# Optimization experiments

Hardware: AMD Instinct MI355X
Metric: run time of the kernel (lower is better)

The kernel has to match this reference:

```python
import jax, jax.numpy as jnp
import numpy as np

B, C, H, W = 32, 192, 32, 32
CH, STRIDE = 8, 2
FEAT = CH * (H // STRIDE) * (W // STRIDE)  # 8*16*16 = 2048


def setup_inputs() -> dict:
    key = jax.random.key(0)
    ks = jax.random.split(key, 7)
    inp = jax.random.normal(ks[0], (B, C, H, W), jnp.float32)
    w_left_out = jax.random.normal(ks[1], (B, C, H, W), jnp.float32)
    conv_w = jax.random.normal(ks[2], (CH, C, 3, 3), jnp.float32) * 0.05
    conv_b = jnp.zeros((CH,), jnp.float32)
    # small scale keeps diag(U) moderate so exp(s) stays finite
    lin_w = jax.random.normal(ks[3], (C * C, FEAT), jnp.float32) * 0.01
    lin_b = jax.random.normal(ks[4], (C * C,), jnp.float32) * 0.1
    s_sign = jnp.sign(jax.random.normal(ks[5], (C,), jnp.float32))
    return dict(inp=inp, w_left_out=w_left_out, conv_w=conv_w, conv_b=conv_b,
                lin_w=lin_w, lin_b=lin_b, s_sign=s_sign)


def _cond_net(x, conv_w, conv_b, lin_w, lin_b):
    # Conv2d(C->CH, k=3, stride=2, pad=1) + ReLU + Flatten + Linear(FEAT -> C*C)
    h = jax.lax.conv_general_dilated(
        x, conv_w, window_strides=(STRIDE, STRIDE), padding=((1, 1), (1, 1)),
        dimension_numbers=('NCHW', 'OIHW', 'NCHW'))
    h = jax.nn.relu(h + conv_b[None, :, None, None])
    return h.reshape(x.shape[0], -1) @ lin_w.T + lin_b  # [B, C*C]


def reference(inp, w_left_out, conv_w, conv_b, lin_w, lin_b, s_sign):
    b, c, height, width = inp.shape
    cond = _cond_net(w_left_out, conv_w, conv_b, lin_w, lin_b)
    mats = cond.reshape(b, c, c)
    # batched LU: a = p @ l @ u (scipy convention, unit-diag l)
    p, l, u = jax.vmap(jax.scipy.linalg.lu)(mats)
    s = jnp.diagonal(u, axis1=1, axis2=2)          # [B, C] raw diag(U)
    eye = jnp.eye(c, dtype=inp.dtype)
    l_full = jnp.tril(l, -1) + eye                  # l * l_mask + I
    u_full = jnp.triu(u, 1) + (s_sign[None, :] * jnp.exp(s))[..., None] * eye
    weight = p @ l_full @ u_full                    # [B, C, C]
    # batched 1x1 conv == per-sample GEMM over spatial positions
    out = jnp.einsum('bij,bjhw->bihw', weight, inp)
    log_w = jnp.mean(jnp.sum(s, axis=1))            # sum(w_s) averaged over batch
    log_det = (height * width) * log_w
    return out, log_det
```

## Files before the change

kernel.cpp:

```cpp
#include <hip/hip_runtime.h>
#include <math.h>


#define NFEAT 2048
#define NN    36864

__global__ __launch_bounds__(256) void conv_kernel(const float* __restrict__ w,
                                                   const float* __restrict__ cw,
                                                   float* __restrict__ hpart) {
  int blk = blockIdx.x;
  int b = blk >> 2, cs = blk & 3;
  int tid = threadIdx.x;
  int oy = tid >> 4, ox = tid & 15;
  __shared__ float wlds[8 * 48 * 9];
  for (int idx = tid; idx < 8 * 48 * 9; idx += 256) {
    int ch = idx / 432, rem = idx - ch * 432;
    int c = rem / 9, kk = rem - c * 9;
    wlds[idx] = cw[ch * 1728 + (cs * 48 + c) * 9 + kk];
  }
  __syncthreads();
  float acc[8];
#pragma unroll
  for (int ch = 0; ch < 8; ++ch) acc[ch] = 0.f;
  const float* img0 = w + (((size_t)b * 192 + cs * 48) << 10);
  for (int c = 0; c < 48; ++c) {
    const float* img = img0 + ((size_t)c << 10);
    float iv[9];
#pragma unroll
    for (int ky = 0; ky < 3; ++ky)
#pragma unroll
      for (int kx = 0; kx < 3; ++kx) {
        int iy = 2 * oy - 1 + ky, ix = 2 * ox - 1 + kx;
        bool ok = (iy >= 0) & (iy < 32) & (ix >= 0) & (ix < 32);
        iv[ky * 3 + kx] = ok ? img[iy * 32 + ix] : 0.f;
      }
#pragma unroll
    for (int ch = 0; ch < 8; ++ch) {
      const float* wp = &wlds[(ch * 48 + c) * 9];
      float s = acc[ch];
#pragma unroll
      for (int t = 0; t < 9; ++t) s = fmaf(iv[t], wp[t], s);
      acc[ch] = s;
    }
  }
  size_t base = ((size_t)(cs * 32 + b) << 11) + tid;
#pragma unroll
  for (int ch = 0; ch < 8; ++ch) hpart[base + (ch << 8)] = acc[ch];
}

__global__ __launch_bounds__(256) void hreduce_kernel(const float* __restrict__ hpart,
                                                      const float* __restrict__ cb,
                                                      float* __restrict__ h_bt) {
  int g = blockIdx.x * 256 + threadIdx.x;
  int k = g & 2047, b = g >> 11;
  float s = 0.f;
#pragma unroll
  for (int cs = 0; cs < 4; ++cs) s += hpart[(((size_t)(cs * 32 + b)) << 11) + k];
  s += cb[k >> 8];
  s = fmaxf(s, 0.f);
  h_bt[g] = s;
}

#define WROW(r) ((r) * 68 + (((r) >> 3) << 2))
__global__ __launch_bounds__(128) void linear_kernel(const float* __restrict__ h_bt,
                                                     const float* __restrict__ lw,
                                                     float* __restrict__ qpart) {
  __shared__ float Wbuf[8768];
  __shared__ float Hbuf[2192];
  int tid = threadIdx.x;
  int blk = blockIdx.x;
  int q = blk & 3;
  int tile = blk >> 2;
  int n0 = tile << 7;
  int kqb = q << 9;
  int bp = tid & 7;
  int ng = tid >> 3;
  int nb = ng << 3;
  int bb0 = bp << 2;
  float acc[32];
#pragma unroll
  for (int i = 0; i < 32; ++i) acc[i] = 0.f;

  for (int kc = 0; kc < 8; ++kc) {
    int koff = kqb + (kc << 6);
#pragma unroll
    for (int j = 0; j < 16; ++j) {
      int f = tid + (j << 7);
      int row = f >> 4, c4 = (f & 15) << 2;
      *(float4*)(Wbuf + WROW(row) + c4) =
          *(const float4*)(lw + (size_t)(n0 + row) * 2048 + koff + c4);
    }
#pragma unroll
    for (int j = 0; j < 4; ++j) {
      int f = tid + (j << 7);
      int bi = f >> 4, c4 = (f & 15) << 2;
      *(float4*)(Hbuf + WROW(bi) + c4) =
          *(const float4*)(h_bt + (size_t)bi * 2048 + koff + c4);
    }
    __syncthreads();
#pragma unroll 2
    for (int k4 = 0; k4 < 16; ++k4) {
      int kk = k4 << 2;
      float4 h0 = *(const float4*)(Hbuf + WROW(bb0 + 0) + kk);
      float4 h1 = *(const float4*)(Hbuf + WROW(bb0 + 1) + kk);
      float4 h2 = *(const float4*)(Hbuf + WROW(bb0 + 2) + kk);
      float4 h3 = *(const float4*)(Hbuf + WROW(bb0 + 3) + kk);
#pragma unroll
      for (int j = 0; j < 8; ++j) {
        float4 w4 = *(const float4*)(Wbuf + WROW(nb + j) + kk);
        float s0 = acc[j * 4 + 0], s1 = acc[j * 4 + 1];
        float s2 = acc[j * 4 + 2], s3 = acc[j * 4 + 3];
        s0 = fmaf(w4.x, h0.x, s0); s0 = fmaf(w4.y, h0.y, s0);
        s0 = fmaf(w4.z, h0.z, s0); s0 = fmaf(w4.w, h0.w, s0);
        s1 = fmaf(w4.x, h1.x, s1); s1 = fmaf(w4.y, h1.y, s1);
        s1 = fmaf(w4.z, h1.z, s1); s1 = fmaf(w4.w, h1.w, s1);
        s2 = fmaf(w4.x, h2.x, s2); s2 = fmaf(w4.y, h2.y, s2);
        s2 = fmaf(w4.z, h2.z, s2); s2 = fmaf(w4.w, h2.w, s2);
        s3 = fmaf(w4.x, h3.x, s3); s3 = fmaf(w4.y, h3.y, s3);
        s3 = fmaf(w4.z, h3.z, s3); s3 = fmaf(w4.w, h3.w, s3);
        acc[j * 4 + 0] = s0; acc[j * 4 + 1] = s1;
        acc[j * 4 + 2] = s2; acc[j * 4 + 3] = s3;
      }
    }
    __syncthreads();
  }
#pragma unroll
  for (int i = 0; i < 4; ++i) {
    float* p = qpart + (size_t)q * 1179648 + (size_t)(bb0 + i) * NN + n0 + nb;
    *(float4*)(p + 0) = make_float4(acc[0 * 4 + i], acc[1 * 4 + i], acc[2 * 4 + i], acc[3 * 4 + i]);
    *(float4*)(p + 4) = make_float4(acc[4 * 4 + i], acc[5 * 4 + i], acc[6 * 4 + i], acc[7 * 4 + i]);
  }
}

__global__ __launch_bounds__(256) void combine_kernel(const float* __restrict__ qpart,
                                                      const float* __restrict__ lb,
                                                      float* __restrict__ mats) {
  int blk = blockIdx.x;
  int b = blk / 18, nt = blk - b * 18;
  int n = (nt << 11) + (threadIdx.x << 3);
  size_t base = (size_t)b * NN + n;
#pragma unroll
  for (int h = 0; h < 2; ++h) {
    float4 q0 = *(const float4*)(qpart + 0 * 1179648 + base + 4 * h);
    float4 q1 = *(const float4*)(qpart + 1 * 1179648 + base + 4 * h);
    float4 q2 = *(const float4*)(qpart + 2 * 1179648 + base + 4 * h);
    float4 q3 = *(const float4*)(qpart + 3 * 1179648 + base + 4 * h);
    float4 bb = *(const float4*)(lb + n + 4 * h);
    float4 o;
    o.x = ((q0.x + q1.x) + q2.x) + q3.x + bb.x;
    o.y = ((q0.y + q1.y) + q2.y) + q3.y + bb.y;
    o.z = ((q0.z + q1.z) + q2.z) + q3.z + bb.z;
    o.w = ((q0.w + q1.w) + q2.w) + q3.w + bb.w;
    *(float4*)(mats + base + 4 * h) = o;
  }
}

#define CAT_(A, B) A##B
#define CAT(A, B) CAT_(A, B)
#define PR_0(R) CAT(pA, R).x
#define PR_1(R) CAT(pA, R).y
#define PR_2(R) CAT(pA, R).z
#define PR_3(R) CAT(pA, R).w
#define PR_4(R) CAT(pB, R).x
#define PR_5(R) CAT(pB, R).y
#define PR_6(R) CAT(pB, R).z
#define PR_7(R) CAT(pB, R).w
#define PR(R, K) CAT(PR_, K)(R)
#define UU_0 uA.x
#define UU_1 uA.y
#define UU_2 uA.z
#define UU_3 uA.w
#define UU_4 uB.x
#define UU_5 uB.y
#define UU_6 uB.z
#define UU_7 uB.w
#define UU(K) CAT(UU_, K)
#define UPDJ(R, J) PR(R, J) = fmaf(-m, UU(J), PR(R, J));
#define TAIL_0(R) UPDJ(R,1) UPDJ(R,2) UPDJ(R,3) UPDJ(R,4) UPDJ(R,5) UPDJ(R,6) UPDJ(R,7)
#define TAIL_1(R) UPDJ(R,2) UPDJ(R,3) UPDJ(R,4) UPDJ(R,5) UPDJ(R,6) UPDJ(R,7)
#define TAIL_2(R) UPDJ(R,3) UPDJ(R,4) UPDJ(R,5) UPDJ(R,6) UPDJ(R,7)
#define TAIL_3(R) UPDJ(R,4) UPDJ(R,5) UPDJ(R,6) UPDJ(R,7)
#define TAIL_4(R) UPDJ(R,5) UPDJ(R,6) UPDJ(R,7)
#define TAIL_5(R) UPDJ(R,6) UPDJ(R,7)
#define TAIL_6(R) UPDJ(R,7)
#define TAIL_7(R)
#define UPDROW(R, KK, kg)                                                      \
  if (CAT(lg, R) > (kg)) {                                                     \
    float m = PR(R, KK) * recip;                                               \
    PR(R, KK) = m;                                                             \
    CAT(TAIL_, KK)(R)                                                          \
  }
#define PSTEP(KK) {                                                            \
  const int kg = kpP + KK;                                                     \
  float bv = -1.f; int br = 0x7fffffff;                                        \
  { float v = fabsf(PR(0,KK)); if (lg0 >= kg && (v > bv || (v == bv && lg0 < br))) { bv = v; br = lg0; } } \
  { float v = fabsf(PR(1,KK)); if (lg1 >= kg && (v > bv || (v == bv && lg1 < br))) { bv = v; br = lg1; } } \
  { float v = fabsf(PR(2,KK)); if (lg2 >= kg && (v > bv || (v == bv && lg2 < br))) { bv = v; br = lg2; } } \
  for (int msk = 1; msk <= 32; msk <<= 1) {                                    \
    float ov = __shfl_xor(bv, msk, 64);                                        \
    int obr = __shfl_xor(br, msk, 64);                                         \
    if (ov > bv || (ov == bv && obr < br)) { bv = ov; br = obr; }              \
  }                                                                            \
  bool own0 = (lg0 == br), own1 = (lg1 == br), own2 = (lg2 == br);             \
  float4 sA = own1 ? pA1 : (own2 ? pA2 : pA0);                                 \
  float4 sB = own1 ? pB1 : (own2 ? pB2 : pB0);                                 \
  int owner = (int)__ffsll(__ballot(own0 | own1 | own2)) - 1;                  \
  float4 uA, uB;                                                               \
  uA.x = __shfl(sA.x, owner); uA.y = __shfl(sA.y, owner);                      \
  uA.z = __shfl(sA.z, owner); uA.w = __shfl(sA.w, owner);                      \
  uB.x = __shfl(sB.x, owner); uB.y = __shfl(sB.y, owner);                      \
  uB.z = __shfl(sB.z, owner); uB.w = __shfl(sB.w, owner);                      \
  float piv = UU(KK);                                                          \
  float recip = 1.0f / piv;                                                    \
  if (tid == 0) {                                                              \
    diagU[kg] = piv;                                                           \
    int t0 = rowmap[kg], t1 = rowmap[br];                                      \
    rowmap[kg] = t1; rowmap[br] = t0;                                          \
  }                                                                            \
  lg0 = (lg0 == kg) ? br : ((lg0 == br) ? kg : lg0);                           \
  lg1 = (lg1 == kg) ? br : ((lg1 == br) ? kg : lg1);                           \
  lg2 = (lg2 == kg) ? br : ((lg2 == br) ? kg : lg2);                           \
  UPDROW(0, KK, kg)                                                            \
  UPDROW(1, KK, kg)                                                            \
  UPDROW(2, KK, kg)                                                            \
}
#define FMA4(D, M, S) {                                                        \
  float mm = (M);                                                              \
  D.x = fmaf(-mm, S.x, D.x); D.y = fmaf(-mm, S.y, D.y);                        \
  D.z = fmaf(-mm, S.z, D.z); D.w = fmaf(-mm, S.w, D.w);                        \
}
#define PANEL(KPV) {                                                           \
  const int kpP = (KPV);                                                       \
  const int pcP = kpP >> 2;                                                    \
  float4 pA0 = As4[tid * 49 + pcP],         pB0 = As4[tid * 49 + pcP + 1];     \
  float4 pA1 = As4[(tid + 64) * 49 + pcP],  pB1 = As4[(tid + 64) * 49 + pcP + 1]; \
  float4 pA2 = As4[(tid + 128) * 49 + pcP], pB2 = As4[(tid + 128) * 49 + pcP + 1]; \
  PSTEP(0) PSTEP(1) PSTEP(2) PSTEP(3) PSTEP(4) PSTEP(5) PSTEP(6) PSTEP(7)     \
  As4[tid * 49 + pcP] = pA0;         As4[tid * 49 + pcP + 1] = pB0;            \
  As4[(tid + 64) * 49 + pcP] = pA1;  As4[(tid + 64) * 49 + pcP + 1] = pB1;     \
  As4[(tid + 128) * 49 + pcP] = pA2; As4[(tid + 128) * 49 + pcP + 1] = pB2;    \
}

__global__ __launch_bounds__(768, 1) void lu_kernel(float* __restrict__ A0,
                                                    const float* __restrict__ ssign,
                                                    float* __restrict__ ssum) {
  __shared__ float4 As4[192 * 49];
  __shared__ int rowmap[192];
  __shared__ float diagU[192];
  __shared__ float4 dval4[48];
  float* dvalf = (float*)dval4;
  int b = blockIdx.x;
  int tid = threadIdx.x;
  float* __restrict__ A = A0 + (size_t)b * NN;

#pragma unroll
  for (int j = 0; j < 12; ++j) {
    int chunk = tid + 768 * j;
    int row = chunk / 48, q = chunk - row * 48;
    As4[row * 49 + q] = *(const float4*)(A + row * 192 + 4 * q);
  }
  for (int i = tid; i < 192; i += 768) rowmap[i] = i;
  __syncthreads();

  int lg0 = tid, lg1 = tid + 64, lg2 = tid + 128;

  if (tid < 64) { PANEL(0) }
  __syncthreads();

  const int qg = tid >> 4;
  const int slot = tid & 15;

  for (int p = 0; p < 23; ++p) {
    const int kp = p << 3;
    const int pc = kp >> 2;
    const int qp1 = pc + 2;

    if (tid >= qp1 && tid < 48) {
      const int q = tid;
      const int ur0 = rowmap[kp + 0], ur1 = rowmap[kp + 1];
      const int ur2 = rowmap[kp + 2], ur3 = rowmap[kp + 3];
      const int ur4 = rowmap[kp + 4], ur5 = rowmap[kp + 5];
      const int ur6 = rowmap[kp + 6], ur7 = rowmap[kp + 7];
      float4 u40 = As4[ur0 * 49 + q], u41 = As4[ur1 * 49 + q];
      float4 u42 = As4[ur2 * 49 + q], u43 = As4[ur3 * 49 + q];
      float4 u44 = As4[ur4 * 49 + q], u45 = As4[ur5 * 49 + q];
      float4 u46 = As4[ur6 * 49 + q], u47 = As4[ur7 * 49 + q];
      { float4 la = As4[ur1 * 49 + pc];
        FMA4(u41, la.x, u40) }
      { float4 la = As4[ur2 * 49 + pc];
        FMA4(u42, la.x, u40) FMA4(u42, la.y, u41) }
      { float4 la = As4[ur3 * 49 + pc];
        FMA4(u43, la.x, u40) FMA4(u43, la.y, u41) FMA4(u43, la.z, u42) }
      { float4 la = As4[ur4 * 49 + pc];
        FMA4(u44, la.x, u40) FMA4(u44, la.y, u41) FMA4(u44, la.z, u42) FMA4(u44, la.w, u43) }
      { float4 la = As4[ur5 * 49 + pc]; float4 lb2 = As4[ur5 * 49 + pc + 1];
        FMA4(u45, la.x, u40) FMA4(u45, la.y, u41) FMA4(u45, la.z, u42) FMA4(u45, la.w, u43)
        FMA4(u45, lb2.x, u44) }
      { float4 la = As4[ur6 * 49 + pc]; float4 lb2 = As4[ur6 * 49 + pc + 1];
        FMA4(u46, la.x, u40) FMA4(u46, la.y, u41) FMA4(u46, la.z, u42) FMA4(u46, la.w, u43)
        FMA4(u46, lb2.x, u44) FMA4(u46, lb2.y, u45) }
      { float4 la = As4[ur7 * 49 + pc]; float4 lb2 = As4[ur7 * 49 + pc + 1];
        FMA4(u47, la.x, u40) FMA4(u47, la.y, u41) FMA4(u47, la.z, u42) FMA4(u47, la.w, u43)
        FMA4(u47, lb2.x, u44) FMA4(u47, lb2.y, u45) FMA4(u47, lb2.z, u46) }
      As4[ur0 * 49 + q] = u40; As4[ur1 * 49 + q] = u41;
      As4[ur2 * 49 + q] = u42; As4[ur3 * 49 + q] = u43;
      As4[ur4 * 49 + q] = u44; As4[ur5 * 49 + q] = u45;
      As4[ur6 * 49 + q] = u46; As4[ur7 * 49 + q] = u47;
    }
    __syncthreads();

    {
      const int col = qp1 + (tid >= 384 ? 1 : 0);
      const int rsl = tid - (tid >= 384 ? 384 : 0);
      const int s = kp + 8 + rsl;
      if (s < 192) {
        const int ua0 = rowmap[kp + 0], ua1 = rowmap[kp + 1];
        const int ua2 = rowmap[kp + 2], ua3 = rowmap[kp + 3];
        const int ua4 = rowmap[kp + 4], ua5 = rowmap[kp + 5];
        const int ua6 = rowmap[kp + 6], ua7 = rowmap[kp + 7];
        float4 u40 = As4[ua0 * 49 + col], u41 = As4[ua1 * 49 + col];
        float4 u42 = As4[ua2 * 49 + col], u43 = As4[ua3 * 49 + col];
        float4 u44 = As4[ua4 * 49 + col], u45 = As4[ua5 * 49 + col];
        float4 u46 = As4[ua6 * 49 + col], u47 = As4[ua7 * 49 + col];
        int phys = rowmap[s];
        float4 la = As4[phys * 49 + pc];
        float4 lb2 = As4[phys * 49 + pc + 1];
        float4 c = As4[phys * 49 + col];
        FMA4(c, la.x, u40) FMA4(c, la.y, u41) FMA4(c, la.z, u42) FMA4(c, la.w, u43)
        FMA4(c, lb2.x, u44) FMA4(c, lb2.y, u45) FMA4(c, lb2.z, u46) FMA4(c, lb2.w, u47)
        As4[phys * 49 + col] = c;
      }
    }
    int php0, php1, php2, php3, php4, php5, php6, php7, php8, php9, php10, php11;
#define SNAP(I) CAT(php, I) = rowmap[slot + (I << 4)];
    SNAP(0) SNAP(1) SNAP(2) SNAP(3) SNAP(4) SNAP(5) SNAP(6)
    SNAP(7) SNAP(8) SNAP(9) SNAP(10) SNAP(11)
#undef SNAP
    __syncthreads();

    if (tid < 64) {
      PANEL(kp + 8)
    } else if (qg >= qp1 + 2) {
      const int q = qg;
      const int ub0 = rowmap[kp + 0], ub1 = rowmap[kp + 1];
      const int ub2 = rowmap[kp + 2], ub3 = rowmap[kp + 3];
      const int ub4 = rowmap[kp + 4], ub5 = rowmap[kp + 5];
      const int ub6 = rowmap[kp + 6], ub7 = rowmap[kp + 7];
      float4 u40 = As4[ub0 * 49 + q], u41 = As4[ub1 * 49 + q];
      float4 u42 = As4[ub2 * 49 + q], u43 = As4[ub3 * 49 + q];
      float4 u44 = As4[ub4 * 49 + q], u45 = As4[ub5 * 49 + q];
      float4 u46 = As4[ub6 * 49 + q], u47 = As4[ub7 * 49 + q];
#define GEMMROW(I) {                                                           \
      int s = slot + (I << 4);                                                 \
      if (s >= kp + 8) {                                                       \
        int phys = CAT(php, I);                                                \
        float4 la = As4[phys * 49 + pc];                                       \
        float4 lb2 = As4[phys * 49 + pc + 1];                                  \
        float4 c = As4[phys * 49 + q];                                         \
        FMA4(c, la.x, u40) FMA4(c, la.y, u41) FMA4(c, la.z, u42) FMA4(c, la.w, u43) \
        FMA4(c, lb2.x, u44) FMA4(c, lb2.y, u45) FMA4(c, lb2.z, u46) FMA4(c, lb2.w, u47) \
        As4[phys * 49 + q] = c;                                                \
      }                                                                        \
    }
      GEMMROW(0) GEMMROW(1) GEMMROW(2) GEMMROW(3) GEMMROW(4) GEMMROW(5)
      GEMMROW(6) GEMMROW(7) GEMMROW(8) GEMMROW(9) GEMMROW(10) GEMMROW(11)
#undef GEMMROW
    }
    __syncthreads();
  }

  if (tid == 0) {
    float s = 0.f;
    for (int i = 0; i < 192; ++i) s += diagU[i];
    ssum[b] = s;
  }
  if (tid < 192) dvalf[tid] = ssign[tid] * expf(diagU[tid]) - diagU[tid];
  __syncthreads();
  {
    const int r = tid >> 2;
    const int tq = tid & 3;
    int i = r;
    int phys = rowmap[r];
    float di = dvalf[i];
    float* __restrict__ G = A + (size_t)phys * 192;
    int qi = i >> 2;
    for (int j = 0; j < 12; ++j) {
      int q = tq + 4 * j;
      if (q > qi) continue;
      float4 g4 = *(float4*)(G + 4 * q);
      float4 a4 = As4[phys * 49 + q];
      float4 d4 = dval4[q];
      if (q == qi) {
        int c0 = 4 * q;
        g4.x = (c0 + 0 < i) ? g4.x + a4.x * d4.x : ((c0 + 0 == i) ? g4.x + di : g4.x);
        g4.y = (c0 + 1 < i) ? g4.y + a4.y * d4.y : ((c0 + 1 == i) ? g4.y + di : g4.y);
        g4.z = (c0 + 2 < i) ? g4.z + a4.z * d4.z : ((c0 + 2 == i) ? g4.z + di : g4.z);
        g4.w = (c0 + 3 < i) ? g4.w + a4.w * d4.w : ((c0 + 3 == i) ? g4.w + di : g4.w);
      } else {
        g4.x += a4.x * d4.x;
        g4.y += a4.y * d4.y;
        g4.z += a4.z * d4.z;
        g4.w += a4.w * d4.w;
      }
      *(float4*)(G + 4 * q) = g4;
    }
  }
}

__global__ __launch_bounds__(256) void out_kernel(const float* __restrict__ wt,
                                                  const float* __restrict__ inp,
                                                  const float* __restrict__ ssum,
                                                  float* __restrict__ out) {
  int blk = blockIdx.x;
  int b = blk / 24, rem = blk % 24;
  int it = rem >> 3, jt = rem & 7;
  int i0 = it << 6, hw0 = jt << 7;
  int tid = threadIdx.x;
  int tx = tid & 31, ty = tid >> 5;
  __shared__ float wlds[64 * 36];
  __shared__ float xlds[32 * 128];
  const float* wb = wt + (size_t)b * NN;
  const float* xb = inp + (((size_t)b * 192) << 10);
  float acc[8][4];
#pragma unroll
  for (int r = 0; r < 8; ++r)
#pragma unroll
    for (int c = 0; c < 4; ++c) acc[r][c] = 0.f;
  for (int kc = 0; kc < 6; ++kc) {
    __syncthreads();
#pragma unroll
    for (int j = 0; j < 2; ++j) {
      int f4 = tid + (j << 8);
      int row = f4 >> 3, c4 = (f4 & 7) << 2;
      float4 v = *(const float4*)(wb + (size_t)(i0 + row) * 192 + (kc << 5) + c4);
      *(float4*)(wlds + row * 36 + c4) = v;
    }
#pragma unroll
    for (int j = 0; j < 4; ++j) {
      int f4 = tid + (j << 8);
      int row = f4 >> 5, c4 = (f4 & 31) << 2;
      float4 v = *(const float4*)(xb + (((size_t)(kc << 5) + row) << 10) + hw0 + c4);
      *(float4*)(xlds + (row << 7) + c4) = v;
    }
    __syncthreads();
#pragma unroll 4
    for (int k = 0; k < 32; ++k) {
      float4 xv = *(const float4*)(xlds + (k << 7) + (tx << 2));
      float wr[8];
#pragma unroll
      for (int r = 0; r < 8; ++r) wr[r] = wlds[(ty * 8 + r) * 36 + k];
#pragma unroll
      for (int r = 0; r < 8; ++r) {
        acc[r][0] = fmaf(wr[r], xv.x, acc[r][0]);
        acc[r][1] = fmaf(wr[r], xv.y, acc[r][1]);
        acc[r][2] = fmaf(wr[r], xv.z, acc[r][2]);
        acc[r][3] = fmaf(wr[r], xv.w, acc[r][3]);
      }
    }
  }
  float* ob = out + (((size_t)b * 192 + i0 + ty * 8) << 10) + hw0 + (tx << 2);
#pragma unroll
  for (int r = 0; r < 8; ++r) {
    float4 v = make_float4(acc[r][0], acc[r][1], acc[r][2], acc[r][3]);
    *(float4*)(ob + ((size_t)r << 10)) = v;
  }
  if (blk == 0 && tid == 0) {
    float s = 0.f;
    for (int i = 0; i < 32; ++i) s += ssum[i];
    out[6291456] = 32.f * s;
  }
}

extern "C" void kernel_launch(void* const* d_in, const int* in_sizes, int n_in,
                              void* d_out, int out_size, void* d_ws, size_t ws_size,
                              hipStream_t stream) {
  const float* inp = (const float*)d_in[0];
  const float* wlo = (const float*)d_in[1];
  const float* cw  = (const float*)d_in[2];
  const float* cb  = (const float*)d_in[3];
  const float* lw  = (const float*)d_in[4];
  const float* lb  = (const float*)d_in[5];
  const float* ss  = (const float*)d_in[6];
  float* out = (float*)d_out;
  float* ws = (float*)d_ws;
  float* hpart = ws;
  float* h_bt  = ws + 262144;
  float* mats  = ws + 327680;
  float* ssum  = ws + 1507328;
  float* qpart = out;
  hipLaunchKernelGGL(conv_kernel,    dim3(128),  dim3(256), 0, stream, wlo, cw, hpart);
  hipLaunchKernelGGL(hreduce_kernel, dim3(256),  dim3(256), 0, stream, hpart, cb, h_bt);
  hipLaunchKernelGGL(linear_kernel,  dim3(1152), dim3(128), 0, stream, h_bt, lw, qpart);
  hipLaunchKernelGGL(combine_kernel, dim3(576),  dim3(256), 0, stream, qpart, lb, mats);
  hipLaunchKernelGGL(lu_kernel,      dim3(32),   dim3(768), 0, stream, mats, ss, ssum);
  hipLaunchKernelGGL(out_kernel,     dim3(768),  dim3(256), 0, stream, mats, inp, ssum, out);
}
```

Measured before the change: 424.4 us.

## Widen blocked LU panel from 8 to 16 columns

```diff
diff --git a/kernel.cpp b/kernel.cpp
--- a/kernel.cpp
+++ b/kernel.cpp
@@ -157,45 +157,69 @@
 
 #define CAT_(A, B) A##B
 #define CAT(A, B) CAT_(A, B)
-#define PR_0(R) CAT(pA, R).x
-#define PR_1(R) CAT(pA, R).y
-#define PR_2(R) CAT(pA, R).z
-#define PR_3(R) CAT(pA, R).w
-#define PR_4(R) CAT(pB, R).x
-#define PR_5(R) CAT(pB, R).y
-#define PR_6(R) CAT(pB, R).z
-#define PR_7(R) CAT(pB, R).w
-#define PR(R, K) CAT(PR_, K)(R)
-#define UU_0 uA.x
-#define UU_1 uA.y
-#define UU_2 uA.z
-#define UU_3 uA.w
-#define UU_4 uB.x
-#define UU_5 uB.y
-#define UU_6 uB.z
-#define UU_7 uB.w
-#define UU(K) CAT(UU_, K)
-#define UPDJ(R, J) PR(R, J) = fmaf(-m, UU(J), PR(R, J));
-#define TAIL_0(R) UPDJ(R,1) UPDJ(R,2) UPDJ(R,3) UPDJ(R,4) UPDJ(R,5) UPDJ(R,6) UPDJ(R,7)
-#define TAIL_1(R) UPDJ(R,2) UPDJ(R,3) UPDJ(R,4) UPDJ(R,5) UPDJ(R,6) UPDJ(R,7)
-#define TAIL_2(R) UPDJ(R,3) UPDJ(R,4) UPDJ(R,5) UPDJ(R,6) UPDJ(R,7)
-#define TAIL_3(R) UPDJ(R,4) UPDJ(R,5) UPDJ(R,6) UPDJ(R,7)
-#define TAIL_4(R) UPDJ(R,5) UPDJ(R,6) UPDJ(R,7)
-#define TAIL_5(R) UPDJ(R,6) UPDJ(R,7)
-#define TAIL_6(R) UPDJ(R,7)
-#define TAIL_7(R)
-#define UPDROW(R, KK, kg)                                                      \
+#define PR16_0(R)  CAT(pA, R).x
+#define PR16_1(R)  CAT(pA, R).y
+#define PR16_2(R)  CAT(pA, R).z
+#define PR16_3(R)  CAT(pA, R).w
+#define PR16_4(R)  CAT(pB, R).x
+#define PR16_5(R)  CAT(pB, R).y
+#define PR16_6(R)  CAT(pB, R).z
+#define PR16_7(R)  CAT(pB, R).w
+#define PR16_8(R)  CAT(pC, R).x
+#define PR16_9(R)  CAT(pC, R).y
+#define PR16_10(R) CAT(pC, R).z
+#define PR16_11(R) CAT(pC, R).w
+#define PR16_12(R) CAT(pD, R).x
+#define PR16_13(R) CAT(pD, R).y
+#define PR16_14(R) CAT(pD, R).z
+#define PR16_15(R) CAT(pD, R).w
+#define PR16(R, K) CAT(PR16_, K)(R)
+#define UU16_0  uA.x
+#define UU16_1  uA.y
+#define UU16_2  uA.z
+#define UU16_3  uA.w
+#define UU16_4  uB.x
+#define UU16_5  uB.y
+#define UU16_6  uB.z
+#define UU16_7  uB.w
+#define UU16_8  uC.x
+#define UU16_9  uC.y
+#define UU16_10 uC.z
+#define UU16_11 uC.w
+#define UU16_12 uD.x
+#define UU16_13 uD.y
+#define UU16_14 uD.z
+#define UU16_15 uD.w
+#define UU16(K) CAT(UU16_, K)
+#define UPDJ16(R, J) PR16(R, J) = fmaf(-m, UU16(J), PR16(R, J));
+#define T16_0(R)  UPDJ16(R,1) UPDJ16(R,2) UPDJ16(R,3) UPDJ16(R,4) UPDJ16(R,5) UPDJ16(R,6) UPDJ16(R,7) UPDJ16(R,8) UPDJ16(R,9) UPDJ16(R,10) UPDJ16(R,11) UPDJ16(R,12) UPDJ16(R,13) UPDJ16(R,14) UPDJ16(R,15)
+#define T16_1(R)  UPDJ16(R,2) UPDJ16(R,3) UPDJ16(R,4) UPDJ16(R,5) UPDJ16(R,6) UPDJ16(R,7) UPDJ16(R,8) UPDJ16(R,9) UPDJ16(R,10) UPDJ16(R,11) UPDJ16(R,12) UPDJ16(R,13) UPDJ16(R,14) UPDJ16(R,15)
+#define T16_2(R)  UPDJ16(R,3) UPDJ16(R,4) UPDJ16(R,5) UPDJ16(R,6) UPDJ16(R,7) UPDJ16(R,8) UPDJ16(R,9) UPDJ16(R,10) UPDJ16(R,11) UPDJ16(R,12) UPDJ16(R,13) UPDJ16(R,14) UPDJ16(R,15)
+#define T16_3(R)  UPDJ16(R,4) UPDJ16(R,5) UPDJ16(R,6) UPDJ16(R,7) UPDJ16(R,8) UPDJ16(R,9) UPDJ16(R,10) UPDJ16(R,11) UPDJ16(R,12) UPDJ16(R,13) UPDJ16(R,14) UPDJ16(R,15)
+#define T16_4(R)  UPDJ16(R,5) UPDJ16(R,6) UPDJ16(R,7) UPDJ16(R,8) UPDJ16(R,9) UPDJ16(R,10) UPDJ16(R,11) UPDJ16(R,12) UPDJ16(R,13) UPDJ16(R,14) UPDJ16(R,15)
+#define T16_5(R)  UPDJ16(R,6) UPDJ16(R,7) UPDJ16(R,8) UPDJ16(R,9) UPDJ16(R,10) UPDJ16(R,11) UPDJ16(R,12) UPDJ16(R,13) UPDJ16(R,14) UPDJ16(R,15)
+#define T16_6(R)  UPDJ16(R,7) UPDJ16(R,8) UPDJ16(R,9) UPDJ16(R,10) UPDJ16(R,11) UPDJ16(R,12) UPDJ16(R,13) UPDJ16(R,14) UPDJ16(R,15)
+#define T16_7(R)  UPDJ16(R,8) UPDJ16(R,9) UPDJ16(R,10) UPDJ16(R,11) UPDJ16(R,12) UPDJ16(R,13) UPDJ16(R,14) UPDJ16(R,15)
+#define T16_8(R)  UPDJ16(R,9) UPDJ16(R,10) UPDJ16(R,11) UPDJ16(R,12) UPDJ16(R,13) UPDJ16(R,14) UPDJ16(R,15)
+#define T16_9(R)  UPDJ16(R,10) UPDJ16(R,11) UPDJ16(R,12) UPDJ16(R,13) UPDJ16(R,14) UPDJ16(R,15)
+#define T16_10(R) UPDJ16(R,11) UPDJ16(R,12) UPDJ16(R,13) UPDJ16(R,14) UPDJ16(R,15)
+#define T16_11(R) UPDJ16(R,12) UPDJ16(R,13) UPDJ16(R,14) UPDJ16(R,15)
+#define T16_12(R) UPDJ16(R,13) UPDJ16(R,14) UPDJ16(R,15)
+#define T16_13(R) UPDJ16(R,14) UPDJ16(R,15)
+#define T16_14(R) UPDJ16(R,15)
+#define T16_15(R)
+#define UPDROW16(R, KK, kg)                                                    \
   if (CAT(lg, R) > (kg)) {                                                     \
-    float m = PR(R, KK) * recip;                                               \
-    PR(R, KK) = m;                                                             \
-    CAT(TAIL_, KK)(R)                                                          \
-  }
-#define PSTEP(KK) {                                                            \
+    float m = PR16(R, KK) * recip;                                             \
+    PR16(R, KK) = m;                                                           \
+    CAT(T16_, KK)(R)                                                           \
+  }
+#define PSTEP16(KK) {                                                          \
   const int kg = kpP + KK;                                                     \
   float bv = -1.f; int br = 0x7fffffff;                                        \
-  { float v = fabsf(PR(0,KK)); if (lg0 >= kg && (v > bv || (v == bv && lg0 < br))) { bv = v; br = lg0; } } \
-  { float v = fabsf(PR(1,KK)); if (lg1 >= kg && (v > bv || (v == bv && lg1 < br))) { bv = v; br = lg1; } } \
-  { float v = fabsf(PR(2,KK)); if (lg2 >= kg && (v > bv || (v == bv && lg2 < br))) { bv = v; br = lg2; } } \
+  { float v = fabsf(PR16(0,KK)); if (lg0 >= kg && (v > bv || (v == bv && lg0 < br))) { bv = v; br = lg0; } } \
+  { float v = fabsf(PR16(1,KK)); if (lg1 >= kg && (v > bv || (v == bv && lg1 < br))) { bv = v; br = lg1; } } \
+  { float v = fabsf(PR16(2,KK)); if (lg2 >= kg && (v > bv || (v == bv && lg2 < br))) { bv = v; br = lg2; } } \
   for (int msk = 1; msk <= 32; msk <<= 1) {                                    \
     float ov = __shfl_xor(bv, msk, 64);                                        \
     int obr = __shfl_xor(br, msk, 64);                                         \
@@ -204,13 +228,19 @@
   bool own0 = (lg0 == br), own1 = (lg1 == br), own2 = (lg2 == br);             \
   float4 sA = own1 ? pA1 : (own2 ? pA2 : pA0);                                 \
   float4 sB = own1 ? pB1 : (own2 ? pB2 : pB0);                                 \
+  float4 sC = own1 ? pC1 : (own2 ? pC2 : pC0);                                 \
+  float4 sD = own1 ? pD1 : (own2 ? pD2 : pD0);                                 \
   int owner = (int)__ffsll(__ballot(own0 | own1 | own2)) - 1;                  \
-  float4 uA, uB;                                                               \
+  float4 uA, uB, uC, uD;                                                       \
   uA.x = __shfl(sA.x, owner); uA.y = __shfl(sA.y, owner);                      \
   uA.z = __shfl(sA.z, owner); uA.w = __shfl(sA.w, owner);                      \
   uB.x = __shfl(sB.x, owner); uB.y = __shfl(sB.y, owner);                      \
   uB.z = __shfl(sB.z, owner); uB.w = __shfl(sB.w, owner);                      \
-  float piv = UU(KK);                                                          \
+  uC.x = __shfl(sC.x, owner); uC.y = __shfl(sC.y, owner);                      \
+  uC.z = __shfl(sC.z, owner); uC.w = __shfl(sC.w, owner);                      \
+  uD.x = __shfl(sD.x, owner); uD.y = __shfl(sD.y, owner);                      \
+  uD.z = __shfl(sD.z, owner); uD.w = __shfl(sD.w, owner);                      \
+  float piv = UU16(KK);                                                        \
   float recip = 1.0f / piv;                                                    \
   if (tid == 0) {                                                              \
     diagU[kg] = piv;                                                           \
@@ -220,26 +250,39 @@
   lg0 = (lg0 == kg) ? br : ((lg0 == br) ? kg : lg0);                           \
   lg1 = (lg1 == kg) ? br : ((lg1 == br) ? kg : lg1);                           \
   lg2 = (lg2 == kg) ? br : ((lg2 == br) ? kg : lg2);                           \
-  UPDROW(0, KK, kg)                                                            \
-  UPDROW(1, KK, kg)                                                            \
-  UPDROW(2, KK, kg)                                                            \
+  UPDROW16(0, KK, kg)                                                          \
+  UPDROW16(1, KK, kg)                                                          \
+  UPDROW16(2, KK, kg)                                                          \
 }
 #define FMA4(D, M, S) {                                                        \
   float mm = (M);                                                              \
   D.x = fmaf(-mm, S.x, D.x); D.y = fmaf(-mm, S.y, D.y);                        \
   D.z = fmaf(-mm, S.z, D.z); D.w = fmaf(-mm, S.w, D.w);                        \
 }
-#define PANEL(KPV) {                                                           \
+#define PANEL16(KPV) {                                                         \
   const int kpP = (KPV);                                                       \
   const int pcP = kpP >> 2;                                                    \
-  float4 pA0 = As4[tid * 49 + pcP],         pB0 = As4[tid * 49 + pcP + 1];     \
-  float4 pA1 = As4[(tid + 64) * 49 + pcP],  pB1 = As4[(tid + 64) * 49 + pcP + 1]; \
-  float4 pA2 = As4[(tid + 128) * 49 + pcP], pB2 = As4[(tid + 128) * 49 + pcP + 1]; \
-  PSTEP(0) PSTEP(1) PSTEP(2) PSTEP(3) PSTEP(4) PSTEP(5) PSTEP(6) PSTEP(7)     \
-  As4[tid * 49 + pcP] = pA0;         As4[tid * 49 + pcP + 1] = pB0;            \
-  As4[(tid + 64) * 49 + pcP] = pA1;  As4[(tid + 64) * 49 + pcP + 1] = pB1;     \
-  As4[(tid + 128) * 49 + pcP] = pA2; As4[(tid + 128) * 49 + pcP + 1] = pB2;    \
-}
+  float4 pA0 = As4[tid * 49 + pcP],           pB0 = As4[tid * 49 + pcP + 1];   \
+  float4 pC0 = As4[tid * 49 + pcP + 2],       pD0 = As4[tid * 49 + pcP + 3];   \
+  float4 pA1 = As4[(tid + 64) * 49 + pcP],    pB1 = As4[(tid + 64) * 49 + pcP + 1]; \
+  float4 pC1 = As4[(tid + 64) * 49 + pcP + 2], pD1 = As4[(tid + 64) * 49 + pcP + 3]; \
+  float4 pA2 = As4[(tid + 128) * 49 + pcP],   pB2 = As4[(tid + 128) * 49 + pcP + 1]; \
+  float4 pC2 = As4[(tid + 128) * 49 + pcP + 2], pD2 = As4[(tid + 128) * 49 + pcP + 3]; \
+  PSTEP16(0) PSTEP16(1) PSTEP16(2) PSTEP16(3) PSTEP16(4) PSTEP16(5)           \
+  PSTEP16(6) PSTEP16(7) PSTEP16(8) PSTEP16(9) PSTEP16(10) PSTEP16(11)         \
+  PSTEP16(12) PSTEP16(13) PSTEP16(14) PSTEP16(15)                             \
+  As4[tid * 49 + pcP] = pA0;           As4[tid * 49 + pcP + 1] = pB0;          \
+  As4[tid * 49 + pcP + 2] = pC0;       As4[tid * 49 + pcP + 3] = pD0;          \
+  As4[(tid + 64) * 49 + pcP] = pA1;    As4[(tid + 64) * 49 + pcP + 1] = pB1;   \
+  As4[(tid + 64) * 49 + pcP + 2] = pC1; As4[(tid + 64) * 49 + pcP + 3] = pD1;  \
+  As4[(tid + 128) * 49 + pcP] = pA2;   As4[(tid + 128) * 49 + pcP + 1] = pB2;  \
+  As4[(tid + 128) * 49 + pcP + 2] = pC2; As4[(tid + 128) * 49 + pcP + 3] = pD2; \
+}
+#define GCHAIN16(c, la, lb2, lc2, ld2)                                         \
+  FMA4(c, la.x, uu0)  FMA4(c, la.y, uu1)  FMA4(c, la.z, uu2)  FMA4(c, la.w, uu3) \
+  FMA4(c, lb2.x, uu4) FMA4(c, lb2.y, uu5) FMA4(c, lb2.z, uu6) FMA4(c, lb2.w, uu7) \
+  FMA4(c, lc2.x, uu8) FMA4(c, lc2.y, uu9) FMA4(c, lc2.z, uu10) FMA4(c, lc2.w, uu11) \
+  FMA4(c, ld2.x, uu12) FMA4(c, ld2.y, uu13) FMA4(c, ld2.z, uu14) FMA4(c, ld2.w, uu15)
 
 __global__ __launch_bounds__(768, 1) void lu_kernel(float* __restrict__ A0,
                                                     const float* __restrict__ ssign,
@@ -264,70 +307,109 @@
 
   int lg0 = tid, lg1 = tid + 64, lg2 = tid + 128;
 
-  if (tid < 64) { PANEL(0) }
+  if (tid < 64) { PANEL16(0) }
   __syncthreads();
 
   const int qg = tid >> 4;
   const int slot = tid & 15;
-
-  for (int p = 0; p < 23; ++p) {
-    const int kp = p << 3;
+  const int colA = tid / 192;
+  const int rA = tid - colA * 192;
+
+  for (int p = 0; p < 11; ++p) {
+    const int kp = p << 4;
     const int pc = kp >> 2;
-    const int qp1 = pc + 2;
+    const int qp1 = pc + 4;
 
     if (tid >= qp1 && tid < 48) {
       const int q = tid;
-      const int ur0 = rowmap[kp + 0], ur1 = rowmap[kp + 1];
-      const int ur2 = rowmap[kp + 2], ur3 = rowmap[kp + 3];
-      const int ur4 = rowmap[kp + 4], ur5 = rowmap[kp + 5];
-      const int ur6 = rowmap[kp + 6], ur7 = rowmap[kp + 7];
-      float4 u40 = As4[ur0 * 49 + q], u41 = As4[ur1 * 49 + q];
-      float4 u42 = As4[ur2 * 49 + q], u43 = As4[ur3 * 49 + q];
-      float4 u44 = As4[ur4 * 49 + q], u45 = As4[ur5 * 49 + q];
-      float4 u46 = As4[ur6 * 49 + q], u47 = As4[ur7 * 49 + q];
+      const int ur0 = rowmap[kp + 0], ur1 = rowmap[kp + 1], ur2 = rowmap[kp + 2], ur3 = rowmap[kp + 3];
+      const int ur4 = rowmap[kp + 4], ur5 = rowmap[kp + 5], ur6 = rowmap[kp + 6], ur7 = rowmap[kp + 7];
+      const int ur8 = rowmap[kp + 8], ur9 = rowmap[kp + 9], ur10 = rowmap[kp + 10], ur11 = rowmap[kp + 11];
+      const int ur12 = rowmap[kp + 12], ur13 = rowmap[kp + 13], ur14 = rowmap[kp + 14], ur15 = rowmap[kp + 15];
+      float4 uu0 = As4[ur0 * 49 + q], uu1 = As4[ur1 * 49 + q], uu2 = As4[ur2 * 49 + q], uu3 = As4[ur3 * 49 + q];
+      float4 uu4 = As4[ur4 * 49 + q], uu5 = As4[ur5 * 49 + q], uu6 = As4[ur6 * 49 + q], uu7 = As4[ur7 * 49 + q];
+      float4 uu8 = As4[ur8 * 49 + q], uu9 = As4[ur9 * 49 + q], uu10 = As4[ur10 * 49 + q], uu11 = As4[ur11 * 49 + q];
+      float4 uu12 = As4[ur12 * 49 + q], uu13 = As4[ur13 * 49 + q], uu14 = As4[ur14 * 49 + q], uu15 = As4[ur15 * 49 + q];
       { float4 la = As4[ur1 * 49 + pc];
-        FMA4(u41, la.x, u40) }
+        FMA4(uu1, la.x, uu0) }
       { float4 la = As4[ur2 * 49 + pc];
-        FMA4(u42, la.x, u40) FMA4(u42, la.y, u41) }
+        FMA4(uu2, la.x, uu0) FMA4(uu2, la.y, uu1) }
       { float4 la = As4[ur3 * 49 + pc];
-        FMA4(u43, la.x, u40) FMA4(u43, la.y, u41) FMA4(u43, la.z, u42) }
+        FMA4(uu3, la.x, uu0) FMA4(uu3, la.y, uu1) FMA4(uu3, la.z, uu2) }
       { float4 la = As4[ur4 * 49 + pc];
-        FMA4(u44, la.x, u40) FMA4(u44, la.y, u41) FMA4(u44, la.z, u42) FMA4(u44, la.w, u43) }
+        FMA4(uu4, la.x, uu0) FMA4(uu4, la.y, uu1) FMA4(uu4, la.z, uu2) FMA4(uu4, la.w, uu3) }
       { float4 la = As4[ur5 * 49 + pc]; float4 lb2 = As4[ur5 * 49 + pc + 1];
-        FMA4(u45, la.x, u40) FMA4(u45, la.y, u41) FMA4(u45, la.z, u42) FMA4(u45, la.w, u43)
-        FMA4(u45, lb2.x, u44) }
+        FMA4(uu5, la.x, uu0) FMA4(uu5, la.y, uu1) FMA4(uu5, la.z, uu2) FMA4(uu5, la.w, uu3)
+        FMA4(uu5, lb2.x, uu4) }
       { float4 la = As4[ur6 * 49 + pc]; float4 lb2 = As4[ur6 * 49 + pc + 1];
-        FMA4(u46, la.x, u40) FMA4(u46, la.y, u41) FMA4(u46, la.z, u42) FMA4(u46, la.w, u43)
-        FMA4(u46, lb2.x, u44) FMA4(u46, lb2.y, u45) }
+        FMA4(uu6, la.x, uu0) FMA4(uu6, la.y, uu1) FMA4(uu6, la.z, uu2) FMA4(uu6, la.w, uu3)
+        FMA4(uu6, lb2.x, uu4) FMA4(uu6, lb2.y, uu5) }
       { float4 la = As4[ur7 * 49 + pc]; float4 lb2 = As4[ur7 * 49 + pc + 1];
-        FMA4(u47, la.x, u40) FMA4(u47, la.y, u41) FMA4(u47, la.z, u42) FMA4(u47, la.w, u43)
-        FMA4(u47, lb2.x, u44) FMA4(u47, lb2.y, u45) FMA4(u47, lb2.z, u46) }
-      As4[ur0 * 49 + q] = u40; As4[ur1 * 49 + q] = u41;
-      As4[ur2 * 49 + q] = u42; As4[ur3 * 49 + q] = u43;
-      As4[ur4 * 49 + q] = u44; As4[ur5 * 49 + q] = u45;
-      As4[ur6 * 49 + q] = u46; As4[ur7 * 49 + q] = u47;
+        FMA4(uu7, la.x, uu0) FMA4(uu7, la.y, uu1) FMA4(uu7, la.z, uu2) FMA4(uu7, la.w, uu3)
+        FMA4(uu7, lb2.x, uu4) FMA4(uu7, lb2.y, uu5) FMA4(uu7, lb2.z, uu6) }
+      { float4 la = As4[ur8 * 49 + pc]; float4 lb2 = As4[ur8 * 49 + pc + 1];
+        FMA4(uu8, la.x, uu0) FMA4(uu8, la.y, uu1) FMA4(uu8, la.z, uu2) FMA4(uu8, la.w, uu3)
+        FMA4(uu8, lb2.x, uu4) FMA4(uu8, lb2.y, uu5) FMA4(uu8, lb2.z, uu6) FMA4(uu8, lb2.w, uu7) }
+      { float4 la = As4[ur9 * 49 + pc]; float4 lb2 = As4[ur9 * 49 + pc + 1]; float4 lc2 = As4[ur9 * 49 + pc + 2];
+        FMA4(uu9, la.x, uu0) FMA4(uu9, la.y, uu1) FMA4(uu9, la.z, uu2) FMA4(uu9, la.w, uu3)
+        FMA4(uu9, lb2.x, uu4) FMA4(uu9, lb2.y, uu5) FMA4(uu9, lb2.z, uu6) FMA4(uu9, lb2.w, uu7)
+        FMA4(uu9, lc2.x, uu8) }
+      { float4 la = As4[ur10 * 49 + pc]; float4 lb2 = As4[ur10 * 49 + pc + 1]; float4 lc2 = As4[ur10 * 49 + pc + 2];
+        FMA4(uu10, la.x, uu0) FMA4(uu10, la.y, uu1) FMA4(uu10, la.z, uu2) FMA4(uu10, la.w, uu3)
+        FMA4(uu10, lb2.x, uu4) FMA4(uu10, lb2.y, uu5) FMA4(uu10, lb2.z, uu6) FMA4(uu10, lb2.w, uu7)
+        FMA4(uu10, lc2.x, uu8) FMA4(uu10, lc2.y, uu9) }
+      { float4 la = As4[ur11 * 49 + pc]; float4 lb2 = As4[ur11 * 49 + pc + 1]; float4 lc2 = As4[ur11 * 49 + pc + 2];
+        FMA4(uu11, la.x, uu0) FMA4(uu11, la.y, uu1) FMA4(uu11, la.z, uu2) FMA4(uu11, la.w, uu3)
+        FMA4(uu11, lb2.x, uu4) FMA4(uu11, lb2.y, uu5) FMA4(uu11, lb2.z, uu6) FMA4(uu11, lb2.w, uu7)
+        FMA4(uu11, lc2.x, uu8) FMA4(uu11, lc2.y, uu9) FMA4(uu11, lc2.z, uu10) }
+      { float4 la = As4[ur12 * 49 + pc]; float4 lb2 = As4[ur12 * 49 + pc + 1]; float4 lc2 = As4[ur12 * 49 + pc + 2];
+        FMA4(uu12, la.x, uu0) FMA4(uu12, la.y, uu1) FMA4(uu12, la.z, uu2) FMA4(uu12, la.w, uu3)
+        FMA4(uu12, lb2.x, uu4) FMA4(uu12, lb2.y, uu5) FMA4(uu12, lb2.z, uu6) FMA4(uu12, lb2.w, uu7)
+        FMA4(uu12, lc2.x, uu8) FMA4(uu12, lc2.y, uu9) FMA4(uu12, lc2.z, uu10) FMA4(uu12, lc2.w, uu11) }
+      { float4 la = As4[ur13 * 49 + pc]; float4 lb2 = As4[ur13 * 49 + pc + 1];
+        float4 lc2 = As4[ur13 * 49 + pc + 2]; float4 ld2 = As4[ur13 * 49 + pc + 3];
+        FMA4(uu13, la.x, uu0) FMA4(uu13, la.y, uu1) FMA4(uu13, la.z, uu2) FMA4(uu13, la.w, uu3)
+        FMA4(uu13, lb2.x, uu4) FMA4(uu13, lb2.y, uu5) FMA4(uu13, lb2.z, uu6) FMA4(uu13, lb2.w, uu7)
+        FMA4(uu13, lc2.x, uu8) FMA4(uu13, lc2.y, uu9) FMA4(uu13, lc2.z, uu10) FMA4(uu13, lc2.w, uu11)
+        FMA4(uu13, ld2.x, uu12) }
+      { float4 la = As4[ur14 * 49 + pc]; float4 lb2 = As4[ur14 * 49 + pc + 1];
+        float4 lc2 = As4[ur14 * 49 + pc + 2]; float4 ld2 = As4[ur14 * 49 + pc + 3];
+        FMA4(uu14, la.x, uu0) FMA4(uu14, la.y, uu1) FMA4(uu14, la.z, uu2) FMA4(uu14, la.w, uu3)
+        FMA4(uu14, lb2.x, uu4) FMA4(uu14, lb2.y, uu5) FMA4(uu14, lb2.z, uu6) FMA4(uu14, lb2.w, uu7)
+        FMA4(uu14, lc2.x, uu8) FMA4(uu14, lc2.y, uu9) FMA4(uu14, lc2.z, uu10) FMA4(uu14, lc2.w, uu11)
+        FMA4(uu14, ld2.x, uu12) FMA4(uu14, ld2.y, uu13) }
+      { float4 la = As4[ur15 * 49 + pc]; float4 lb2 = As4[ur15 * 49 + pc + 1];
+        float4 lc2 = As4[ur15 * 49 + pc + 2]; float4 ld2 = As4[ur15 * 49 + pc + 3];
+        FMA4(uu15, la.x, uu0) FMA4(uu15, la.y, uu1) FMA4(uu15, la.z, uu2) FMA4(uu15, la.w, uu3)
+        FMA4(uu15, lb2.x, uu4) FMA4(uu15, lb2.y, uu5) FMA4(uu15, lb2.z, uu6) FMA4(uu15, lb2.w, uu7)
+        FMA4(uu15, lc2.x, uu8) FMA4(uu15, lc2.y, uu9) FMA4(uu15, lc2.z, uu10) FMA4(uu15, lc2.w, uu11)
+        FMA4(uu15, ld2.x, uu12) FMA4(uu15, ld2.y, uu13) FMA4(uu15, ld2.z, uu14) }
+      As4[ur0 * 49 + q] = uu0;  As4[ur1 * 49 + q] = uu1;  As4[ur2 * 49 + q] = uu2;  As4[ur3 * 49 + q] = uu3;
+      As4[ur4 * 49 + q] = uu4;  As4[ur5 * 49 + q] = uu5;  As4[ur6 * 49 + q] = uu6;  As4[ur7 * 49 + q] = uu7;
+      As4[ur8 * 49 + q] = uu8;  As4[ur9 * 49 + q] = uu9;  As4[ur10 * 49 + q] = uu10; As4[ur11 * 49 + q] = uu11;
+      As4[ur12 * 49 + q] = uu12; As4[ur13 * 49 + q] = uu13; As4[ur14 * 49 + q] = uu14; As4[ur15 * 49 + q] = uu15;
     }
     __syncthreads();
 
     {
-      const int col = qp1 + (tid >= 384 ? 1 : 0);
-      const int rsl = tid - (tid >= 384 ? 384 : 0);
-      const int s = kp + 8 + rsl;
+      const int col = qp1 + colA;
+      const int s = kp + 16 + rA;
       if (s < 192) {
-        const int ua0 = rowmap[kp + 0], ua1 = rowmap[kp + 1];
-        const int ua2 = rowmap[kp + 2], ua3 = rowmap[kp + 3];
-        const int ua4 = rowmap[kp + 4], ua5 = rowmap[kp + 5];
-        const int ua6 = rowmap[kp + 6], ua7 = rowmap[kp + 7];
-        float4 u40 = As4[ua0 * 49 + col], u41 = As4[ua1 * 49 + col];
-        float4 u42 = As4[ua2 * 49 + col], u43 = As4[ua3 * 49 + col];
-        float4 u44 = As4[ua4 * 49 + col], u45 = As4[ua5 * 49 + col];
-        float4 u46 = As4[ua6 * 49 + col], u47 = As4[ua7 * 49 + col];
+        const int ua0 = rowmap[kp + 0], ua1 = rowmap[kp + 1], ua2 = rowmap[kp + 2], ua3 = rowmap[kp + 3];
+        const int ua4 = rowmap[kp + 4], ua5 = rowmap[kp + 5], ua6 = rowmap[kp + 6], ua7 = rowmap[kp + 7];
+        const int ua8 = rowmap[kp + 8], ua9 = rowmap[kp + 9], ua10 = rowmap[kp + 10], ua11 = rowmap[kp + 11];
+        const int ua12 = rowmap[kp + 12], ua13 = rowmap[kp + 13], ua14 = rowmap[kp + 14], ua15 = rowmap[kp + 15];
+        float4 uu0 = As4[ua0 * 49 + col], uu1 = As4[ua1 * 49 + col], uu2 = As4[ua2 * 49 + col], uu3 = As4[ua3 * 49 + col];
+        float4 uu4 = As4[ua4 * 49 + col], uu5 = As4[ua5 * 49 + col], uu6 = As4[ua6 * 49 + col], uu7 = As4[ua7 * 49 + col];
+        float4 uu8 = As4[ua8 * 49 + col], uu9 = As4[ua9 * 49 + col], uu10 = As4[ua10 * 49 + col], uu11 = As4[ua11 * 49 + col];
+        float4 uu12 = As4[ua12 * 49 + col], uu13 = As4[ua13 * 49 + col], uu14 = As4[ua14 * 49 + col], uu15 = As4[ua15 * 49 + col];
         int phys = rowmap[s];
         float4 la = As4[phys * 49 + pc];
         float4 lb2 = As4[phys * 49 + pc + 1];
+        float4 lc2 = As4[phys * 49 + pc + 2];
+        float4 ld2 = As4[phys * 49 + pc + 3];
         float4 c = As4[phys * 49 + col];
-        FMA4(c, la.x, u40) FMA4(c, la.y, u41) FMA4(c, la.z, u42) FMA4(c, la.w, u43)
-        FMA4(c, lb2.x, u44) FMA4(c, lb2.y, u45) FMA4(c, lb2.z, u46) FMA4(c, lb2.w, u47)
+        GCHAIN16(c, la, lb2, lc2, ld2)
         As4[phys * 49 + col] = c;
       }
     }
@@ -339,32 +421,33 @@
     __syncthreads();
 
     if (tid < 64) {
-      PANEL(kp + 8)
-    } else if (qg >= qp1 + 2) {
+      PANEL16(kp + 16)
+    } else if (qg >= qp1 + 4) {
       const int q = qg;
-      const int ub0 = rowmap[kp + 0], ub1 = rowmap[kp + 1];
-      const int ub2 = rowmap[kp + 2], ub3 = rowmap[kp + 3];
-      const int ub4 = rowmap[kp + 4], ub5 = rowmap[kp + 5];
-      const int ub6 = rowmap[kp + 6], ub7 = rowmap[kp + 7];
-      float4 u40 = As4[ub0 * 49 + q], u41 = As4[ub1 * 49 + q];
-      float4 u42 = As4[ub2 * 49 + q], u43 = As4[ub3 * 49 + q];
-      float4 u44 = As4[ub4 * 49 + q], u45 = As4[ub5 * 49 + q];
-      float4 u46 = As4[ub6 * 49 + q], u47 = As4[ub7 * 49 + q];
-#define GEMMROW(I) {                                                           \
+      const int ub0 = rowmap[kp + 0], ub1 = rowmap[kp + 1], ub2 = rowmap[kp + 2], ub3 = rowmap[kp + 3];
+      const int ub4 = rowmap[kp + 4], ub5 = rowmap[kp + 5], ub6 = rowmap[kp + 6], ub7 = rowmap[kp + 7];
+      const int ub8 = rowmap[kp + 8], ub9 = rowmap[kp + 9], ub10 = rowmap[kp + 10], ub11 = rowmap[kp + 11];
+      const int ub12 = rowmap[kp + 12], ub13 = rowmap[kp + 13], ub14 = rowmap[kp + 14], ub15 = rowmap[kp + 15];
+      float4 uu0 = As4[ub0 * 49 + q], uu1 = As4[ub1 * 49 + q], uu2 = As4[ub2 * 49 + q], uu3 = As4[ub3 * 49 + q];
+      float4 uu4 = As4[ub4 * 49 + q], uu5 = As4[ub5 * 49 + q], uu6 = As4[ub6 * 49 + q], uu7 = As4[ub7 * 49 + q];
+      float4 uu8 = As4[ub8 * 49 + q], uu9 = As4[ub9 * 49 + q], uu10 = As4[ub10 * 49 + q], uu11 = As4[ub11 * 49 + q];
+      float4 uu12 = As4[ub12 * 49 + q], uu13 = As4[ub13 * 49 + q], uu14 = As4[ub14 * 49 + q], uu15 = As4[ub15 * 49 + q];
+#define GEMMROW16(I) {                                                         \
       int s = slot + (I << 4);                                                 \
-      if (s >= kp + 8) {                                                       \
+      if (s >= kp + 16) {                                                      \
         int phys = CAT(php, I);                                                \
         float4 la = As4[phys * 49 + pc];                                       \
         float4 lb2 = As4[phys * 49 + pc + 1];                                  \
+        float4 lc2 = As4[phys * 49 + pc + 2];                                  \
+        float4 ld2 = As4[phys * 49 + pc + 3];                                  \
         float4 c = As4[phys * 49 + q];                                         \
-        FMA4(c, la.x, u40) FMA4(c, la.y, u41) FMA4(c, la.z, u42) FMA4(c, la.w, u43) \
-        FMA4(c, lb2.x, u44) FMA4(c, lb2.y, u45) FMA4(c, lb2.z, u46) FMA4(c, lb2.w, u47) \
+        GCHAIN16(c, la, lb2, lc2, ld2)                                         \
         As4[phys * 49 + q] = c;                                                \
       }                                                                        \
     }
-      GEMMROW(0) GEMMROW(1) GEMMROW(2) GEMMROW(3) GEMMROW(4) GEMMROW(5)
-      GEMMROW(6) GEMMROW(7) GEMMROW(8) GEMMROW(9) GEMMROW(10) GEMMROW(11)
-#undef GEMMROW
+      GEMMROW16(0) GEMMROW16(1) GEMMROW16(2) GEMMROW16(3) GEMMROW16(4) GEMMROW16(5)
+      GEMMROW16(6) GEMMROW16(7) GEMMROW16(8) GEMMROW16(9) GEMMROW16(10) GEMMROW16(11)
+#undef GEMMROW16
     }
     __syncthreads();
   }
```

New measurement: 438.1 us. 3.2% more time.
